# Kernel tuning notes

Measured on AMD Instinct MI355X. Metric: run time of the kernel, lower is better.

The kernel has to match this reference:

```python
import jax, jax.numpy as jnp
import numpy as np

HID = 512
HEADS = 8
D = HID // HEADS          # att_size = 64
B = 64                    # number of graphs
L = 1024                  # bonds per graph (equal-length scopes)
SCALE = D ** (-0.5)
EPS = 1e-5


def setup_inputs() -> dict:
    key = jax.random.key(0)
    ks = jax.random.split(key, 9)
    f = lambda k, s, sc=1.0: jax.random.normal(k, s, dtype=jnp.float32) * sc
    edge_attr = f(ks[0], (B * L, HID))
    # contiguous equal-length scopes: (start, length) per graph
    scopes = np.stack([np.arange(B, dtype=np.int64) * L,
                       np.full(B, L, dtype=np.int64)], axis=1)
    return {
        "edge_attr": edge_attr,
        "batch_scopes": jnp.asarray(scopes),
        "Wq": f(ks[1], (HID, HID), 0.03),   # torch Linear weight [out, in]
        "Wk": f(ks[2], (HID, HID), 0.03),
        "Wv": f(ks[3], (HID, HID), 0.03),
        "Wr": f(ks[4], (D, D), 0.1),
        "w_alpha": f(ks[5], (D,)),
        "w_beta": f(ks[6], (D,)),
        "Wo": f(ks[7], (HID, HID), 0.03),
        "bo": jnp.zeros((HID,), jnp.float32),
        "ln_g": jnp.ones((HID,), jnp.float32),
        "ln_b": jnp.zeros((HID,), jnp.float32),
    }


def reference(edge_attr, batch_scopes, Wq, Wk, Wv, Wr, w_alpha, w_beta,
              Wo, bo, ln_g, ln_b):
    # Scopes are contiguous, equal length L -> pad_sequence == reshape
    padded = edge_attr.reshape(B, L, HID)

    def proj(W):  # (B, L, HID) @ W.T -> (B, heads, L, D)
        return jnp.einsum('blh,dh->bld', padded, W).reshape(B, L, HEADS, D).transpose(0, 2, 1, 3)

    b_q = proj(Wq)
    b_k = proj(Wk)
    b_v = proj(Wv)

    # softmax over the head-feature dim (faithful to dim=-1 in torch code)
    alpha = jax.nn.softmax(b_q * w_alpha * SCALE, axis=-1)
    global_q = jnp.sum(alpha * b_q, axis=2)            # (B, heads, D), sum over L

    p = global_q[:, :, None, :] * b_k                  # (B, heads, L, D)
    beta = jax.nn.softmax(p * w_beta * SCALE, axis=-1)
    global_k = jnp.sum(beta * p, axis=2)               # (B, heads, D)

    kv = global_k[:, :, None, :] * b_v                 # (B, heads, L, D)
    kv_out = jnp.einsum('bhld,ed->bhle', kv, Wr)
    att = jax.nn.relu(kv_out + b_q)                    # dropout p=0 (eval)

    att = att.transpose(0, 2, 1, 3).reshape(B, L, HID)
    out = jnp.einsum('blh,oh->blo', att, Wo) + bo

    # LayerNorm over last dim
    mu = jnp.mean(out, axis=-1, keepdims=True)
    var = jnp.mean((out - mu) ** 2, axis=-1, keepdims=True)
    out = (out - mu) * jax.lax.rsqrt(var + EPS) * ln_g + ln_b

    # unpad + concat == flatten for equal-length contiguous scopes
    return out.reshape(B * L, HID)
```

## Files before the change

kernel.cpp:

```cpp
#include <hip/hip_runtime.h>
#include <stdint.h>


#define SCALE_F 0.125f
#define EPSF 1e-5f

typedef __attribute__((ext_vector_type(8))) short short8;
typedef __attribute__((ext_vector_type(4))) float float4v;
typedef unsigned short ushort_t;

__device__ __forceinline__ ushort_t f2bf(float f) {
  uint32_t u = __builtin_bit_cast(uint32_t, f);
  u += 0x7fffu + ((u >> 16) & 1u);
  return (ushort_t)(u >> 16);
}
__device__ __forceinline__ float bf2f(ushort_t s) {
  uint32_t u = ((uint32_t)s) << 16;
  return __builtin_bit_cast(float, u);
}

__device__ __forceinline__ void gload16(const void* g, void* l) {
  __builtin_amdgcn_global_load_lds(
      (__attribute__((address_space(1))) char*)(char*)const_cast<void*>(g),
      (__attribute__((address_space(3))) char*)(char*)l, 16, 0, 0);
}

#define SBAR() __builtin_amdgcn_s_barrier()
#define LGKM0() do { __builtin_amdgcn_sched_barrier(0);                 \
                     asm volatile("s_waitcnt lgkmcnt(0)" ::: "memory"); \
                     __builtin_amdgcn_sched_barrier(0); } while (0)

__global__ __launch_bounds__(256) void cvt_all(const float* __restrict__ X,
                                               const float* __restrict__ Wq,
                                               const float* __restrict__ Wk,
                                               const float* __restrict__ Wv,
                                               const float* __restrict__ Wo,
                                               ushort_t* __restrict__ Xb,
                                               ushort_t* __restrict__ Wqkv,
                                               ushort_t* __restrict__ Wob) {
  const int i = blockIdx.x * 256 + threadIdx.x;
  if (i < 4194304) {
    const float4v* src = (const float4v*)X;
    float4v v0 = src[(size_t)i * 2];
    float4v v1 = src[(size_t)i * 2 + 1];
    short8 o;
#pragma unroll
    for (int j = 0; j < 4; ++j) {
      o[j]     = (short)f2bf(v0[j]);
      o[j + 4] = (short)f2bf(v1[j]);
    }
    ((short8*)Xb)[i] = o;
  } else {
    const int j = i - 4194304;
    if (j < 262144)        Wqkv[j] = f2bf(Wq[j]);
    else if (j < 524288)   Wqkv[j] = f2bf(Wk[j - 262144]);
    else if (j < 786432)   Wqkv[j] = f2bf(Wv[j - 524288]);
    else                   Wob[j - 786432] = f2bf(Wo[j - 786432]);
  }
}

__global__ __launch_bounds__(512, 2) void gemm8p(const ushort_t* __restrict__ A,
                                                 const ushort_t* __restrict__ Bm,
                                                 ushort_t* __restrict__ C) {
  __shared__ __align__(16) char ldsA[65536];
  __shared__ __align__(16) char ldsB[65536];
  const int swz = (blockIdx.x & 7) * 192 + (blockIdx.x >> 3);
  const int tm = swz / 6, tn = swz % 6;
  const int row0 = tm * 256, col0 = tn * 256;
  const int tid = threadIdx.x, wid = tid >> 6, lane = tid & 63;
  const int wr = wid >> 2, wc = wid & 3;
  const int lr = lane & 15, lk = lane >> 4;
  const int xr = (lr & 7) << 4;

  auto stageA = [&](int t) {
    const int kt = t;
#pragma unroll
    for (int i = 0; i < 4; ++i) {
      const int o = i * 8192 + wid * 1024 + lane * 16;
      const int r = o >> 7, x = o & 127;
      gload16((const char*)A + (size_t)(row0 + r) * 1024 + kt * 128 + (x ^ ((r & 7) << 4)),
              ldsA + (t & 1) * 32768 + i * 8192 + wid * 1024);
    }
  };
  auto stageB = [&](int t) {
    const int kt = t;
#pragma unroll
    for (int i = 0; i < 4; ++i) {
      const int o = i * 8192 + wid * 1024 + lane * 16;
      const int r = o >> 7, x = o & 127;
      gload16((const char*)Bm + (size_t)(col0 + r) * 1024 + kt * 128 + (x ^ ((r & 7) << 4)),
              ldsB + (t & 1) * 32768 + i * 8192 + wid * 1024);
    }
  };
  auto rdA = [&](int sl, int mi, int kk) -> short8 {
    return *(const short8*)(ldsA + sl * 32768 + (wr * 128 + mi * 16 + lr) * 128 +
                            ((kk * 64 + lk * 16) ^ xr));
  };
  auto rdB = [&](int sl, int ni, int kk) -> short8 {
    return *(const short8*)(ldsB + sl * 32768 + (wc * 64 + ni * 16 + lr) * 128 +
                            ((kk * 64 + lk * 16) ^ xr));
  };

  float4v acc[8][4] = {};

  stageA(0); stageB(0);
  stageA(1); stageB(1);
  asm volatile("s_waitcnt vmcnt(8)" ::: "memory");
  SBAR();

#pragma unroll
  for (int t = 0; t < 8; ++t) {
    const int sl = t & 1;
    short8 a0[4][2], a1[4][2], b[4][2];
#pragma unroll
    for (int mi = 0; mi < 4; ++mi)
#pragma unroll
      for (int kk = 0; kk < 2; ++kk) a0[mi][kk] = rdA(sl, mi, kk);
#pragma unroll
    for (int ni = 0; ni < 4; ++ni)
#pragma unroll
      for (int kk = 0; kk < 2; ++kk) b[ni][kk] = rdB(sl, ni, kk);
    LGKM0();
    SBAR();
    if (t + 2 < 8) stageB(t + 2);
#pragma unroll
    for (int mi = 0; mi < 4; ++mi)
#pragma unroll
      for (int kk = 0; kk < 2; ++kk) a1[mi][kk] = rdA(sl, mi + 4, kk);
    __builtin_amdgcn_s_setprio(1);
#pragma unroll
    for (int kk = 0; kk < 2; ++kk)
#pragma unroll
      for (int mi = 0; mi < 4; ++mi)
#pragma unroll
        for (int ni = 0; ni < 4; ++ni)
          acc[mi][ni] = __builtin_amdgcn_mfma_f32_16x16x32_bf16(a0[mi][kk], b[ni][kk], acc[mi][ni], 0, 0, 0);
    __builtin_amdgcn_s_setprio(0);
    LGKM0();
    SBAR();
    if (t + 2 < 8) stageA(t + 2);
    __builtin_amdgcn_s_setprio(1);
#pragma unroll
    for (int kk = 0; kk < 2; ++kk)
#pragma unroll
      for (int mi = 0; mi < 4; ++mi)
#pragma unroll
        for (int ni = 0; ni < 4; ++ni)
          acc[mi + 4][ni] = __builtin_amdgcn_mfma_f32_16x16x32_bf16(a1[mi][kk], b[ni][kk], acc[mi + 4][ni], 0, 0, 0);
    __builtin_amdgcn_s_setprio(0);
    __builtin_amdgcn_sched_barrier(0);
    if (t < 6) {
      asm volatile("s_waitcnt vmcnt(8)" ::: "memory");
    } else if (t == 6) {
      asm volatile("s_waitcnt vmcnt(0)" ::: "memory");
    }
    SBAR();
  }

#pragma unroll
  for (int mi = 0; mi < 8; ++mi)
#pragma unroll
    for (int ni = 0; ni < 4; ++ni) {
      const int col = col0 + wc * 64 + ni * 16 + lr;
#pragma unroll
      for (int r = 0; r < 4; ++r) {
        const int row = row0 + wr * 128 + mi * 16 + lk * 4 + r;
        C[(size_t)row * 1536 + col] = f2bf(acc[mi][ni][r]);
      }
    }
}

__global__ __launch_bounds__(256) void reduce_gq(const ushort_t* __restrict__ QKV,
                                                 const float* __restrict__ w_alpha,
                                                 float* __restrict__ gq_part) {
  const int bx = blockIdx.x, bh = bx >> 2, ch = bx & 3;
  const int b = bh >> 3, h = bh & 7;
  const int tid = threadIdx.x, wid = tid >> 6, lane = tid & 63;
  const int rsub = lane >> 3, dch = lane & 7;
  __shared__ float red[4][64];
  float wa[8];
#pragma unroll
  for (int j = 0; j < 8; ++j) wa[j] = w_alpha[dch * 8 + j] * SCALE_F;
  const size_t base = (size_t)b * 1024 + ch * 256;
  float acc[8] = {0, 0, 0, 0, 0, 0, 0, 0};
  for (int it = 0; it < 8; ++it) {
    const size_t t = base + it * 32 + wid * 8 + rsub;
    short8 raw = *(const short8*)(QKV + t * 1536 + h * 64 + dch * 8);
    float q[8], s[8];
#pragma unroll
    for (int j = 0; j < 8; ++j) { q[j] = bf2f((ushort_t)raw[j]); s[j] = q[j] * wa[j]; }
    float m = s[0];
#pragma unroll
    for (int j = 1; j < 8; ++j) m = fmaxf(m, s[j]);
    m = fmaxf(m, __shfl_xor(m, 1)); m = fmaxf(m, __shfl_xor(m, 2)); m = fmaxf(m, __shfl_xor(m, 4));
    float e[8], sum = 0.f;
#pragma unroll
    for (int j = 0; j < 8; ++j) { e[j] = __expf(s[j] - m); sum += e[j]; }
    sum += __shfl_xor(sum, 1); sum += __shfl_xor(sum, 2); sum += __shfl_xor(sum, 4);
    const float inv = 1.0f / sum;
#pragma unroll
    for (int j = 0; j < 8; ++j) acc[j] += e[j] * inv * q[j];
  }
#pragma unroll
  for (int msk = 8; msk < 64; msk <<= 1)
#pragma unroll
    for (int j = 0; j < 8; ++j) acc[j] += __shfl_xor(acc[j], msk);
  if (lane < 8) {
#pragma unroll
    for (int j = 0; j < 8; ++j) red[wid][lane * 8 + j] = acc[j];
  }
  __syncthreads();
  if (tid < 64)
    gq_part[(size_t)bx * 64 + tid] = red[0][tid] + red[1][tid] + red[2][tid] + red[3][tid];
}

__global__ __launch_bounds__(256) void reduce_gk(const ushort_t* __restrict__ QKV,
                                                 const float* __restrict__ w_beta,
                                                 const float* __restrict__ gq_part,
                                                 float* __restrict__ gk_part) {
  const int bx = blockIdx.x, bh = bx >> 2, ch = bx & 3;
  const int b = bh >> 3, h = bh & 7;
  const int tid = threadIdx.x, wid = tid >> 6, lane = tid & 63;
  const int rsub = lane >> 3, dch = lane & 7;
  __shared__ float red[4][64];
  __shared__ float gq_s[64];
  if (tid < 64) {
    float s = 0.f;
#pragma unroll
    for (int c = 0; c < 4; ++c) s += gq_part[(size_t)(bh * 4 + c) * 64 + tid];
    gq_s[tid] = s;
  }
  __syncthreads();
  float wb[8], gq[8];
#pragma unroll
  for (int j = 0; j < 8; ++j) {
    wb[j] = w_beta[dch * 8 + j] * SCALE_F;
    gq[j] = gq_s[dch * 8 + j];
  }
  const size_t base = (size_t)b * 1024 + ch * 256;
  float acc[8] = {0, 0, 0, 0, 0, 0, 0, 0};
  for (int it = 0; it < 8; ++it) {
    const size_t t = base + it * 32 + wid * 8 + rsub;
    short8 raw = *(const short8*)(QKV + t * 1536 + 512 + h * 64 + dch * 8);
    float p[8], s[8];
#pragma unroll
    for (int j = 0; j < 8; ++j) { p[j] = gq[j] * bf2f((ushort_t)raw[j]); s[j] = p[j] * wb[j]; }
    float m = s[0];
#pragma unroll
    for (int j = 1; j < 8; ++j) m = fmaxf(m, s[j]);
    m = fmaxf(m, __shfl_xor(m, 1)); m = fmaxf(m, __shfl_xor(m, 2)); m = fmaxf(m, __shfl_xor(m, 4));
    float e[8], sum = 0.f;
#pragma unroll
    for (int j = 0; j < 8; ++j) { e[j] = __expf(s[j] - m); sum += e[j]; }
    sum += __shfl_xor(sum, 1); sum += __shfl_xor(sum, 2); sum += __shfl_xor(sum, 4);
    const float inv = 1.0f / sum;
#pragma unroll
    for (int j = 0; j < 8; ++j) acc[j] += e[j] * inv * p[j];
  }
#pragma unroll
  for (int msk = 8; msk < 64; msk <<= 1)
#pragma unroll
    for (int j = 0; j < 8; ++j) acc[j] += __shfl_xor(acc[j], msk);
  if (lane < 8) {
#pragma unroll
    for (int j = 0; j < 8; ++j) red[wid][lane * 8 + j] = acc[j];
  }
  __syncthreads();
  if (tid < 64)
    gk_part[(size_t)bx * 64 + tid] = red[0][tid] + red[1][tid] + red[2][tid] + red[3][tid];
}

__global__ __launch_bounds__(256) void att_k(const ushort_t* __restrict__ QKV,
                                             const float* __restrict__ Wr,
                                             const float* __restrict__ gk_part,
                                             ushort_t* __restrict__ att) {
  const int bx = blockIdx.x, bh = bx >> 2, tc = bx & 3;
  const int b = bh >> 3, h = bh & 7;
  const int tid = threadIdx.x, wid = tid >> 6, lane = tid & 63;
  __shared__ float gk_s[64];
  __shared__ __align__(16) ushort_t Ml[64 * 72];
  if (tid < 64) {
    float s = 0.f;
#pragma unroll
    for (int c = 0; c < 4; ++c) s += gk_part[(size_t)(bh * 4 + c) * 64 + tid];
    gk_s[tid] = s;
  }
  __syncthreads();
  for (int i = tid; i < 4096; i += 256) {
    const int e = i >> 6, d = i & 63;
    Ml[e * 72 + d] = f2bf(Wr[i] * gk_s[d]);
  }
  __syncthreads();
  const int lr = lane & 15, lk = lane >> 4;
  short8 bfr[4][2], bfi[4][2];
#pragma unroll
  for (int ni = 0; ni < 4; ++ni)
#pragma unroll
    for (int ks = 0; ks < 2; ++ks) {
      bfr[ni][ks] = *(const short8*)&Ml[(ni * 16 + lr) * 72 + ks * 32 + lk * 8];
#pragma unroll
      for (int j = 0; j < 8; ++j)
        bfi[ni][ks][j] = (ni * 16 + lr == ks * 32 + lk * 8 + j) ? (short)0x3F80 : (short)0;
    }
  const size_t tw = (size_t)b * 1024 + tc * 256 + wid * 64;
  float4v oacc[4][4] = {};
#pragma unroll
  for (int ks = 0; ks < 2; ++ks) {
    short8 a[4], aq[4];
#pragma unroll
    for (int mi = 0; mi < 4; ++mi) {
      const size_t t = tw + mi * 16 + lr;
      a[mi]  = *(const short8*)(QKV + t * 1536 + 1024 + h * 64 + ks * 32 + lk * 8);
      aq[mi] = *(const short8*)(QKV + t * 1536 +        h * 64 + ks * 32 + lk * 8);
    }
#pragma unroll
    for (int mi = 0; mi < 4; ++mi)
#pragma unroll
      for (int ni = 0; ni < 4; ++ni) {
        oacc[mi][ni] = __builtin_amdgcn_mfma_f32_16x16x32_bf16(a[mi],  bfr[ni][ks], oacc[mi][ni], 0, 0, 0);
        oacc[mi][ni] = __builtin_amdgcn_mfma_f32_16x16x32_bf16(aq[mi], bfi[ni][ks], oacc[mi][ni], 0, 0, 0);
      }
  }
#pragma unroll
  for (int mi = 0; mi < 4; ++mi)
#pragma unroll
    for (int ni = 0; ni < 4; ++ni)
#pragma unroll
      for (int r = 0; r < 4; ++r) {
        const size_t t = tw + mi * 16 + lk * 4 + r;
        const int e = ni * 16 + lr;
        att[t * 512 + h * 64 + e] = f2bf(fmaxf(oacc[mi][ni][r], 0.0f));
      }
}

__global__ __launch_bounds__(512, 2) void gemm_ln(const ushort_t* __restrict__ A,
                                                  const ushort_t* __restrict__ Bm,
                                                  float* __restrict__ out,
                                                  const float* __restrict__ bo,
                                                  const float* __restrict__ lng,
                                                  const float* __restrict__ lnb) {
  __shared__ __align__(16) ushort_t As[2][128 * 32];
  __shared__ __align__(16) ushort_t Bs[2][512 * 32];
  __shared__ float red_s[4][128][2];
  __shared__ float tot_s[128][2];
  const int tid = threadIdx.x, wid = tid >> 6, lane = tid & 63;
  const int wr = wid >> 2, wc = wid & 3;
  const int lr = lane & 15, lk = lane >> 4;
  const int row0 = blockIdx.x * 128;
  float4v acc[4][8] = {};

  const int la = lane * 16;
  const int ar = wid * 16 + (lane >> 2);
  const int acb = (lane & 3) * 16;

  auto stage = [&](int buf, int s) {
    const int k0b = s * 64;
    gload16((const char*)A + (size_t)(row0 + ar) * 1024 + k0b + acb,
            (char*)&As[buf][0] + wid * 1024);
#pragma unroll
    for (int i = 0; i < 4; ++i) {
      const int dst = (wid * 4 + i) * 1024;
      const int br = (dst + la) >> 6;
      const int bcb = la & 63;
      gload16((const char*)Bm + (size_t)br * 1024 + k0b + bcb,
              (char*)&Bs[buf][0] + dst);
    }
  };

  stage(0, 0);
  __syncthreads();
  for (int s = 0; s < 16; ++s) {
    const int buf = s & 1;
    if (s < 15) stage(buf ^ 1, s + 1);
    short8 af[4], bf[8];
#pragma unroll
    for (int mi = 0; mi < 4; ++mi)
      af[mi] = *(const short8*)((const char*)&As[buf][0] + (wr * 64 + mi * 16 + lr) * 64 + lk * 16);
#pragma unroll
    for (int ni = 0; ni < 8; ++ni)
      bf[ni] = *(const short8*)((const char*)&Bs[buf][0] + (wc * 128 + ni * 16 + lr) * 64 + lk * 16);
#pragma unroll
    for (int mi = 0; mi < 4; ++mi)
#pragma unroll
      for (int ni = 0; ni < 8; ++ni)
        acc[mi][ni] = __builtin_amdgcn_mfma_f32_16x16x32_bf16(af[mi], bf[ni], acc[mi][ni], 0, 0, 0);
    __syncthreads();
  }

  float bov[8], gv[8], bv[8];
#pragma unroll
  for (int ni = 0; ni < 8; ++ni) {
    const int c = wc * 128 + ni * 16 + lr;
    bov[ni] = bo[c]; gv[ni] = lng[c]; bv[ni] = lnb[c];
  }
#pragma unroll
  for (int mi = 0; mi < 4; ++mi)
#pragma unroll
    for (int ni = 0; ni < 8; ++ni)
#pragma unroll
      for (int r = 0; r < 4; ++r)
        acc[mi][ni][r] += bov[ni];
#pragma unroll
  for (int mi = 0; mi < 4; ++mi)
#pragma unroll
    for (int r = 0; r < 4; ++r) {
      float s = 0.f, q = 0.f;
#pragma unroll
      for (int ni = 0; ni < 8; ++ni) { const float v = acc[mi][ni][r]; s += v; q += v * v; }
      s += __shfl_xor(s, 1); q += __shfl_xor(q, 1);
      s += __shfl_xor(s, 2); q += __shfl_xor(q, 2);
      s += __shfl_xor(s, 4); q += __shfl_xor(q, 4);
      s += __shfl_xor(s, 8); q += __shfl_xor(q, 8);
      if (lr == 0) {
        const int rb = wr * 64 + mi * 16 + lk * 4 + r;
        red_s[wc][rb][0] = s;
        red_s[wc][rb][1] = q;
      }
    }
  __syncthreads();
  if (tid < 128) {
    tot_s[tid][0] = red_s[0][tid][0] + red_s[1][tid][0] + red_s[2][tid][0] + red_s[3][tid][0];
    tot_s[tid][1] = red_s[0][tid][1] + red_s[1][tid][1] + red_s[2][tid][1] + red_s[3][tid][1];
  }
  __syncthreads();
#pragma unroll
  for (int mi = 0; mi < 4; ++mi)
#pragma unroll
    for (int r = 0; r < 4; ++r) {
      const int rb = wr * 64 + mi * 16 + lk * 4 + r;
      const float mu = tot_s[rb][0] * (1.f / 512.f);
      const float var = tot_s[rb][1] * (1.f / 512.f) - mu * mu;
      const float rs = rsqrtf(var + EPSF);
      float* op = out + (size_t)(row0 + rb) * 512 + wc * 128 + lr;
#pragma unroll
      for (int ni = 0; ni < 8; ++ni)
        op[ni * 16] = (acc[mi][ni][r] - mu) * rs * gv[ni] + bv[ni];
    }
}

extern "C" void kernel_launch(void* const* d_in, const int* in_sizes, int n_in,
                              void* d_out, int out_size, void* d_ws, size_t ws_size,
                              hipStream_t stream) {
  const float* X       = (const float*)d_in[0];
  const float* Wq      = (const float*)d_in[2];
  const float* Wk      = (const float*)d_in[3];
  const float* Wv      = (const float*)d_in[4];
  const float* Wr      = (const float*)d_in[5];
  const float* w_alpha = (const float*)d_in[6];
  const float* w_beta  = (const float*)d_in[7];
  const float* Wo      = (const float*)d_in[8];
  const float* bo      = (const float*)d_in[9];
  const float* ln_g    = (const float*)d_in[10];
  const float* ln_b    = (const float*)d_in[11];

  char* ws = (char*)d_ws;
  ushort_t* Xb      = (ushort_t*)(ws);
  ushort_t* Wqkv    = (ushort_t*)(ws + 67108864);
  ushort_t* Wob     = (ushort_t*)(ws + 68681728);
  ushort_t* QKV     = (ushort_t*)(ws + 69206016);
  float*    gq_part = (float*)(ws + 270532608);
  float*    gk_part = (float*)(ws + 271056896);
  ushort_t* att     = Xb;
  float* out = (float*)d_out;

  hipLaunchKernelGGL(cvt_all, dim3(20480), dim3(256), 0, stream,
                     X, Wq, Wk, Wv, Wo, Xb, Wqkv, Wob);
  hipLaunchKernelGGL(gemm8p, dim3(1536), dim3(512), 0, stream, Xb, Wqkv, QKV);
  hipLaunchKernelGGL(reduce_gq, dim3(2048), dim3(256), 0, stream, QKV, w_alpha, gq_part);
  hipLaunchKernelGGL(reduce_gk, dim3(2048), dim3(256), 0, stream,
                     QKV, w_beta, gq_part, gk_part);
  hipLaunchKernelGGL(att_k, dim3(2048), dim3(256), 0, stream, QKV, Wr, gk_part, att);
  hipLaunchKernelGGL(gemm_ln, dim3(512), dim3(512), 0, stream,
                     att, Wob, out, bo, ln_g, ln_b);
}
```

Before: 326.2 us.

## Fuse attention kernel into output GEMM+LayerNorm via LDS-resident att tile

Merges the per-head Wr projection/ReLU kernel with the output projection GEMM and LayerNorm. Each 512-thread block computes the bf16 attention activations for 128 tokens across all 8 heads into shared memory, then runs the Wo GEMM from LDS. The Wo operand is read directly from global memory rather than through staged, double-buffered LDS. This removes the global write and re-read of the 64 MB att intermediate and one launch, at the cost of about 133 KB of LDS per block, which lowers occupancy. The Wo loads now go straight to registers with no prefetch pipelining.

After: 325.2 us, median of 3. About the same (-0.3%).

```diff
diff --git a/kernel.cpp b/kernel.cpp
--- a/kernel.cpp
+++ b/kernel.cpp
@@ -270,121 +270,100 @@
     gk_part[(size_t)bx * 64 + tid] = red[0][tid] + red[1][tid] + red[2][tid] + red[3][tid];
 }
 
-__global__ __launch_bounds__(256) void att_k(const ushort_t* __restrict__ QKV,
-                                             const float* __restrict__ Wr,
-                                             const float* __restrict__ gk_part,
-                                             ushort_t* __restrict__ att) {
-  const int bx = blockIdx.x, bh = bx >> 2, tc = bx & 3;
-  const int b = bh >> 3, h = bh & 7;
+__global__ __launch_bounds__(512, 2) void att_out(const ushort_t* __restrict__ QKV,
+                                                  const float* __restrict__ Wr,
+                                                  const float* __restrict__ gk_part,
+                                                  const ushort_t* __restrict__ Wob,
+                                                  const float* __restrict__ bo,
+                                                  const float* __restrict__ lng,
+                                                  const float* __restrict__ lnb,
+                                                  float* __restrict__ out) {
+  __shared__ __align__(16) ushort_t att_s[128 * 520];
+  __shared__ float gk_s[8][64];
+  __shared__ float red_s[4][128][2];
+  __shared__ float tot_s[128][2];
+  const int bx = blockIdx.x;
+  const int t0 = bx * 128;
+  const int bg = bx >> 3;
   const int tid = threadIdx.x, wid = tid >> 6, lane = tid & 63;
-  __shared__ float gk_s[64];
-  __shared__ __align__(16) ushort_t Ml[64 * 72];
-  if (tid < 64) {
+  const int lr = lane & 15, lk = lane >> 4;
+
+  {
+    const int h = tid >> 6, d = tid & 63;
+    const int bh = bg * 8 + h;
     float s = 0.f;
 #pragma unroll
-    for (int c = 0; c < 4; ++c) s += gk_part[(size_t)(bh * 4 + c) * 64 + tid];
-    gk_s[tid] = s;
-  }
-  __syncthreads();
-  for (int i = tid; i < 4096; i += 256) {
-    const int e = i >> 6, d = i & 63;
-    Ml[e * 72 + d] = f2bf(Wr[i] * gk_s[d]);
-  }
-  __syncthreads();
-  const int lr = lane & 15, lk = lane >> 4;
-  short8 bfr[4][2], bfi[4][2];
+    for (int c = 0; c < 4; ++c) s += gk_part[(size_t)(bh * 4 + c) * 64 + d];
+    gk_s[h][d] = s;
+  }
+  __syncthreads();
+
+  short8 bfi[4][2];
 #pragma unroll
   for (int ni = 0; ni < 4; ++ni)
 #pragma unroll
-    for (int ks = 0; ks < 2; ++ks) {
-      bfr[ni][ks] = *(const short8*)&Ml[(ni * 16 + lr) * 72 + ks * 32 + lk * 8];
+    for (int ks = 0; ks < 2; ++ks)
 #pragma unroll
       for (int j = 0; j < 8; ++j)
         bfi[ni][ks][j] = (ni * 16 + lr == ks * 32 + lk * 8 + j) ? (short)0x3F80 : (short)0;
-    }
-  const size_t tw = (size_t)b * 1024 + tc * 256 + wid * 64;
-  float4v oacc[4][4] = {};
-#pragma unroll
-  for (int ks = 0; ks < 2; ++ks) {
-    short8 a[4], aq[4];
-#pragma unroll
-    for (int mi = 0; mi < 4; ++mi) {
-      const size_t t = tw + mi * 16 + lr;
-      a[mi]  = *(const short8*)(QKV + t * 1536 + 1024 + h * 64 + ks * 32 + lk * 8);
-      aq[mi] = *(const short8*)(QKV + t * 1536 +        h * 64 + ks * 32 + lk * 8);
-    }
+
+  const size_t trow = (size_t)t0 + wid * 16 + lr;
+  for (int h = 0; h < 8; ++h) {
+    short8 bfr[4][2];
+#pragma unroll
+    for (int ni = 0; ni < 4; ++ni)
+#pragma unroll
+      for (int ks = 0; ks < 2; ++ks) {
+        const int e = ni * 16 + lr;
+        const int k0 = ks * 32 + lk * 8;
+        const float4v w0 = *(const float4v*)(Wr + e * 64 + k0);
+        const float4v w1 = *(const float4v*)(Wr + e * 64 + k0 + 4);
+        const float4v g0 = *(const float4v*)(&gk_s[h][k0]);
+        const float4v g1 = *(const float4v*)(&gk_s[h][k0 + 4]);
+        short8 rfrag;
+#pragma unroll
+        for (int j = 0; j < 4; ++j) {
+          rfrag[j]     = (short)f2bf(w0[j] * g0[j]);
+          rfrag[j + 4] = (short)f2bf(w1[j] * g1[j]);
+        }
+        bfr[ni][ks] = rfrag;
+      }
+    float4v pacc[4] = {};
+#pragma unroll
+    for (int ks = 0; ks < 2; ++ks) {
+      const short8 av  = *(const short8*)(QKV + trow * 1536 + 1024 + h * 64 + ks * 32 + lk * 8);
+      const short8 aqv = *(const short8*)(QKV + trow * 1536 +        h * 64 + ks * 32 + lk * 8);
+#pragma unroll
+      for (int ni = 0; ni < 4; ++ni) {
+        pacc[ni] = __builtin_amdgcn_mfma_f32_16x16x32_bf16(av,  bfr[ni][ks], pacc[ni], 0, 0, 0);
+        pacc[ni] = __builtin_amdgcn_mfma_f32_16x16x32_bf16(aqv, bfi[ni][ks], pacc[ni], 0, 0, 0);
+      }
+    }
+#pragma unroll
+    for (int ni = 0; ni < 4; ++ni)
+#pragma unroll
+      for (int r = 0; r < 4; ++r)
+        att_s[(wid * 16 + lk * 4 + r) * 520 + h * 64 + ni * 16 + lr] =
+            f2bf(fmaxf(pacc[ni][r], 0.0f));
+  }
+  __syncthreads();
+
+  const int wr = wid >> 2, wc = wid & 3;
+  float4v acc[4][8] = {};
+#pragma unroll 4
+  for (int kc = 0; kc < 16; ++kc) {
+    short8 a[4], bf[8];
 #pragma unroll
     for (int mi = 0; mi < 4; ++mi)
-#pragma unroll
-      for (int ni = 0; ni < 4; ++ni) {
-        oacc[mi][ni] = __builtin_amdgcn_mfma_f32_16x16x32_bf16(a[mi],  bfr[ni][ks], oacc[mi][ni], 0, 0, 0);
-        oacc[mi][ni] = __builtin_amdgcn_mfma_f32_16x16x32_bf16(aq[mi], bfi[ni][ks], oacc[mi][ni], 0, 0, 0);
-      }
-  }
-#pragma unroll
-  for (int mi = 0; mi < 4; ++mi)
-#pragma unroll
-    for (int ni = 0; ni < 4; ++ni)
-#pragma unroll
-      for (int r = 0; r < 4; ++r) {
-        const size_t t = tw + mi * 16 + lk * 4 + r;
-        const int e = ni * 16 + lr;
-        att[t * 512 + h * 64 + e] = f2bf(fmaxf(oacc[mi][ni][r], 0.0f));
-      }
-}
-
-__global__ __launch_bounds__(512, 2) void gemm_ln(const ushort_t* __restrict__ A,
-                                                  const ushort_t* __restrict__ Bm,
-                                                  float* __restrict__ out,
-                                                  const float* __restrict__ bo,
-                                                  const float* __restrict__ lng,
-                                                  const float* __restrict__ lnb) {
-  __shared__ __align__(16) ushort_t As[2][128 * 32];
-  __shared__ __align__(16) ushort_t Bs[2][512 * 32];
-  __shared__ float red_s[4][128][2];
-  __shared__ float tot_s[128][2];
-  const int tid = threadIdx.x, wid = tid >> 6, lane = tid & 63;
-  const int wr = wid >> 2, wc = wid & 3;
-  const int lr = lane & 15, lk = lane >> 4;
-  const int row0 = blockIdx.x * 128;
-  float4v acc[4][8] = {};
-
-  const int la = lane * 16;
-  const int ar = wid * 16 + (lane >> 2);
-  const int acb = (lane & 3) * 16;
-
-  auto stage = [&](int buf, int s) {
-    const int k0b = s * 64;
-    gload16((const char*)A + (size_t)(row0 + ar) * 1024 + k0b + acb,
-            (char*)&As[buf][0] + wid * 1024);
-#pragma unroll
-    for (int i = 0; i < 4; ++i) {
-      const int dst = (wid * 4 + i) * 1024;
-      const int br = (dst + la) >> 6;
-      const int bcb = la & 63;
-      gload16((const char*)Bm + (size_t)br * 1024 + k0b + bcb,
-              (char*)&Bs[buf][0] + dst);
-    }
-  };
-
-  stage(0, 0);
-  __syncthreads();
-  for (int s = 0; s < 16; ++s) {
-    const int buf = s & 1;
-    if (s < 15) stage(buf ^ 1, s + 1);
-    short8 af[4], bf[8];
+      a[mi] = *(const short8*)(att_s + (wr * 64 + mi * 16 + lr) * 520 + kc * 32 + lk * 8);
+#pragma unroll
+    for (int ni = 0; ni < 8; ++ni)
+      bf[ni] = *(const short8*)(Wob + (size_t)(wc * 128 + ni * 16 + lr) * 512 + kc * 32 + lk * 8);
 #pragma unroll
     for (int mi = 0; mi < 4; ++mi)
-      af[mi] = *(const short8*)((const char*)&As[buf][0] + (wr * 64 + mi * 16 + lr) * 64 + lk * 16);
-#pragma unroll
-    for (int ni = 0; ni < 8; ++ni)
-      bf[ni] = *(const short8*)((const char*)&Bs[buf][0] + (wc * 128 + ni * 16 + lr) * 64 + lk * 16);
-#pragma unroll
-    for (int mi = 0; mi < 4; ++mi)
 #pragma unroll
       for (int ni = 0; ni < 8; ++ni)
-        acc[mi][ni] = __builtin_amdgcn_mfma_f32_16x16x32_bf16(af[mi], bf[ni], acc[mi][ni], 0, 0, 0);
-    __syncthreads();
+        acc[mi][ni] = __builtin_amdgcn_mfma_f32_16x16x32_bf16(a[mi], bf[ni], acc[mi][ni], 0, 0, 0);
   }
 
   float bov[8], gv[8], bv[8];
@@ -431,7 +410,7 @@
       const float mu = tot_s[rb][0] * (1.f / 512.f);
       const float var = tot_s[rb][1] * (1.f / 512.f) - mu * mu;
       const float rs = rsqrtf(var + EPSF);
-      float* op = out + (size_t)(row0 + rb) * 512 + wc * 128 + lr;
+      float* op = out + (size_t)(t0 + rb) * 512 + wc * 128 + lr;
 #pragma unroll
       for (int ni = 0; ni < 8; ++ni)
         op[ni * 16] = (acc[mi][ni][r] - mu) * rs * gv[ni] + bv[ni];
@@ -460,7 +439,6 @@
   ushort_t* QKV     = (ushort_t*)(ws + 69206016);
   float*    gq_part = (float*)(ws + 270532608);
   float*    gk_part = (float*)(ws + 271056896);
-  ushort_t* att     = Xb;
   float* out = (float*)d_out;
 
   hipLaunchKernelGGL(cvt_all, dim3(20480), dim3(256), 0, stream,
@@ -469,7 +447,6 @@
   hipLaunchKernelGGL(reduce_gq, dim3(2048), dim3(256), 0, stream, QKV, w_alpha, gq_part);
   hipLaunchKernelGGL(reduce_gk, dim3(2048), dim3(256), 0, stream,
                      QKV, w_beta, gq_part, gk_part);
-  hipLaunchKernelGGL(att_k, dim3(2048), dim3(256), 0, stream, QKV, Wr, gk_part, att);
-  hipLaunchKernelGGL(gemm_ln, dim3(512), dim3(512), 0, stream,
-                     att, Wob, out, bo, ln_g, ln_b);
-}
+  hipLaunchKernelGGL(att_out, dim3(512), dim3(512), 0, stream,
+                     QKV, Wr, gk_part, Wob, bo, ln_g, ln_b, out);
+}
```
